# Performance work log

Measured on AMD Instinct MI355X. Metric: run time of the kernel, lower is better.

Reference implementation:

```python
import jax, jax.numpy as jnp
import numpy as np

I_DECAY = 0.95
STAG_THRESH = 0.95
MAX_GATE = 0.6
MIN_I_GATE = 0.25
EPS = 1e-12


def setup_inputs() -> dict:
    key = jax.random.key(0)
    ks = jax.random.split(key, 9)
    B, T, D_IN, D_OUT = 4, 2048, 2048, 2048
    x = jax.random.normal(ks[0], (B, T, D_IN), dtype=jnp.float32)
    s = 1.0 / np.sqrt(D_IN)
    Wp = jax.random.uniform(ks[1], (D_IN, D_OUT), jnp.float32, -s, s)
    Wi = jax.random.uniform(ks[2], (D_IN, D_OUT), jnp.float32, -s, s) * 0.3
    Wd = jax.random.uniform(ks[3], (D_IN, D_OUT), jnp.float32, -s, s) * 0.3
    gate_w = jax.random.uniform(ks[4], (D_IN, 3), jnp.float32, -s, s)
    gate_b = jnp.array([0.5, 0.0, 0.0], dtype=jnp.float32)
    kick_vec = jax.random.normal(ks[5], (D_OUT,), dtype=jnp.float32) * 0.01
    kick_w = jax.random.uniform(ks[6], (D_IN, 1), jnp.float32, -s, s)
    kick_b = jnp.full((1,), -2.0, dtype=jnp.float32)
    bias = jnp.zeros((D_OUT,), dtype=jnp.float32)
    return {"x": x, "Wp": Wp, "Wi": Wi, "Wd": Wd, "gate_w": gate_w,
            "gate_b": gate_b, "kick_vec": kick_vec, "kick_w": kick_w,
            "kick_b": kick_b, "bias": bias}


def _ema_integral(x, decay):
    # x: [B,T,D] -> time-major scan; integral[0] = x[0]
    xt = jnp.swapaxes(x, 0, 1)  # [T,B,D]

    def step(carry, xcur):
        new = decay * carry + (1.0 - decay) * xcur
        return new, new

    init = xt[0]
    _, rest = jax.lax.scan(step, init, xt[1:])
    integral = jnp.concatenate([init[None], rest], axis=0)
    return jnp.swapaxes(integral, 0, 1)  # [B,T,D]


def reference(x, Wp, Wi, Wd, gate_w, gate_b, kick_vec, kick_w, kick_b, bias):
    B, T, D = x.shape
    # --- EMA integral (linear recurrence over T) ---
    integral = _ema_integral(x, I_DECAY)

    # --- stagnation-aware derivative ---
    diff = jnp.concatenate(
        [jnp.zeros_like(x[:, :1]), x[:, 1:] - x[:, :-1]], axis=1)
    x_norm = x / jnp.maximum(
        jnp.linalg.norm(x, axis=-1, keepdims=True), EPS)
    cos_sim = jnp.concatenate(
        [jnp.zeros((B, 1), x.dtype),
         jnp.sum(x_norm[:, 1:] * x_norm[:, :-1], axis=-1)], axis=1)  # [B,T]
    stagnation = (cos_sim > STAG_THRESH).astype(x.dtype)
    kick_strength = jax.nn.sigmoid(
        jnp.einsum('btd,do->bto', x, kick_w) + kick_b)[..., 0]  # [B,T]
    derivative = diff + (stagnation * kick_strength)[..., None] * kick_vec

    # --- gates: softmax -> clamp max -> clamp I min -> renormalize ---
    g = jax.nn.softmax(jnp.einsum('btd,dg->btg', x, gate_w) + gate_b, axis=-1)
    g = jnp.minimum(g, MAX_GATE)
    g = g.at[..., 1].set(jnp.maximum(g[..., 1], MIN_I_GATE))
    g = g / jnp.sum(g, axis=-1, keepdims=True)

    out = (g[..., 0:1] * jnp.einsum('btd,do->bto', x, Wp)
           + g[..., 1:2] * jnp.einsum('btd,do->bto', integral, Wi)
           + g[..., 2:3] * jnp.einsum('btd,do->bto', derivative, Wd))
    return out + bias
```

## Files before the change

### kernel.cpp

```cpp
#include <hip/hip_runtime.h>

#define DH 2048
#define TT 2048
#define BB 4
#define MROWS 8192
#define NZ 6144
#define NCH 128
#define LCH 16
#define LAM 0.44012667f
#define LAM2 1.982646e-06f

typedef __attribute__((ext_vector_type(8))) short bf16x8;
typedef __attribute__((ext_vector_type(4))) float f32x4;

__device__ __forceinline__ unsigned short f2bf(float f) {
  union { float f; unsigned int u; } v; v.f = f;
  unsigned int u = v.u;
  return (unsigned short)((u + 0x7FFFu + ((u >> 16) & 1u)) >> 16);
}
__device__ __forceinline__ float bf2f(unsigned short u) {
  union { unsigned int i; float f; } v; v.i = ((unsigned int)u) << 16;
  return v.f;
}
__device__ __forceinline__ void gld16(const unsigned short* g, unsigned short* l) {
  __builtin_amdgcn_global_load_lds((const __attribute__((address_space(1))) void*)g,
                                   (__attribute__((address_space(3))) void*)l, 16, 0, 0);
}

__global__ __launch_bounds__(256) void prep_w(const float* __restrict__ Wp,
                                              const float* __restrict__ Wi,
                                              const float* __restrict__ Wd,
                                              const float* __restrict__ kick_vec,
                                              unsigned short* __restrict__ Wt,
                                              float* __restrict__ kvWd) {
  __shared__ float tile[64][65];
  int bid = blockIdx.x;
  int mat = bid >> 10;
  int t2 = bid & 1023;
  int dt = (t2 >> 5) * 64;
  int ot = (t2 & 31) * 64;
  const float* W = (mat == 0) ? Wp : ((mat == 1) ? Wi : Wd);
  int nbase = mat * DH;
  int tid = threadIdx.x;
  int r = tid >> 4;
  int c4 = (tid & 15) * 4;
#pragma unroll
  for (int i = 0; i < 4; ++i) {
    int rr = r + i * 16;
    float4 v = *(const float4*)&W[(size_t)(dt + rr) * DH + ot + c4];
    tile[rr][c4 + 0] = v.x; tile[rr][c4 + 1] = v.y;
    tile[rr][c4 + 2] = v.z; tile[rr][c4 + 3] = v.w;
  }
  __syncthreads();
  int o = tid >> 3;
  int d8 = (tid & 7) * 8;
#pragma unroll
  for (int pass = 0; pass < 2; ++pass) {
    int oo = o + pass * 32;
    union { unsigned short u[8]; uint4 v; } pk;
#pragma unroll
    for (int i = 0; i < 8; ++i) pk.u[i] = f2bf(tile[d8 + i][oo]);
    *(uint4*)&Wt[(size_t)(nbase + ot + oo) * DH + dt + d8] = pk.v;
  }
  if (mat == 2 && tid < 64) {
    float s = 0.f;
#pragma unroll 8
    for (int dd = 0; dd < 64; ++dd) s += kick_vec[dt + dd] * tile[dd][tid];
    atomicAdd(&kvWd[ot + tid], s);
  }
}

__global__ __launch_bounds__(256) void conv_x(const float* __restrict__ x,
                                              const float* __restrict__ gate_w,
                                              const float* __restrict__ gate_b,
                                              const float* __restrict__ kick_w,
                                              const float* __restrict__ kick_b,
                                              float* __restrict__ rs,
                                              unsigned short* __restrict__ A) {
  int r = blockIdx.x;
  int t = r & (TT - 1);
  const float* xr = x + (size_t)r * DH;
  const float* xq = xr - DH;
  const bool hp = (t != 0);
  int tid = threadIdx.x;
  float a0 = 0, a1 = 0, a2 = 0, ak = 0, axx = 0, apx = 0, app = 0;
#pragma unroll
  for (int it = 0; it < 2; ++it) {
    int d0 = (tid + it * 256) * 4;
    float4 xv = *(const float4*)(xr + d0);
    float4 pv = hp ? *(const float4*)(xq + d0) : make_float4(0.f, 0.f, 0.f, 0.f);
    float4 q0 = *(const float4*)(gate_w + (size_t)d0 * 3);
    float4 q1 = *(const float4*)(gate_w + (size_t)d0 * 3 + 4);
    float4 q2 = *(const float4*)(gate_w + (size_t)d0 * 3 + 8);
    float4 kw = *(const float4*)(kick_w + d0);
    float xa[4] = {xv.x, xv.y, xv.z, xv.w};
    float pa[4] = {pv.x, pv.y, pv.z, pv.w};
    a0 += xa[0] * q0.x + xa[1] * q0.w + xa[2] * q1.z + xa[3] * q2.y;
    a1 += xa[0] * q0.y + xa[1] * q1.x + xa[2] * q1.w + xa[3] * q2.z;
    a2 += xa[0] * q0.z + xa[1] * q1.y + xa[2] * q2.x + xa[3] * q2.w;
    ak += xa[0] * kw.x + xa[1] * kw.y + xa[2] * kw.z + xa[3] * kw.w;
    union { unsigned short u[4]; uint2 v; } pk;
#pragma unroll
    for (int j = 0; j < 4; ++j) {
      axx += xa[j] * xa[j];
      apx += xa[j] * pa[j];
      app += pa[j] * pa[j];
      pk.u[j] = f2bf(xa[j]);
    }
    *(uint2*)&A[(size_t)r * DH + d0] = pk.v;
  }
#pragma unroll
  for (int off = 32; off > 0; off >>= 1) {
    a0 += __shfl_xor(a0, off); a1 += __shfl_xor(a1, off);
    a2 += __shfl_xor(a2, off); ak += __shfl_xor(ak, off);
    axx += __shfl_xor(axx, off); apx += __shfl_xor(apx, off);
    app += __shfl_xor(app, off);
  }
  __shared__ float red[4][7];
  int wv = tid >> 6;
  if ((tid & 63) == 0) {
    red[wv][0] = a0; red[wv][1] = a1; red[wv][2] = a2; red[wv][3] = ak;
    red[wv][4] = axx; red[wv][5] = apx; red[wv][6] = app;
  }
  __syncthreads();
  if (tid == 0) {
    float v[7];
#pragma unroll
    for (int i = 0; i < 7; ++i) v[i] = red[0][i] + red[1][i] + red[2][i] + red[3][i];
    float l0 = v[0] + gate_b[0], l1 = v[1] + gate_b[1], l2 = v[2] + gate_b[2];
    float mx = fmaxf(l0, fmaxf(l1, l2));
    float e0 = expf(l0 - mx), e1 = expf(l1 - mx), e2 = expf(l2 - mx);
    float inv = 1.f / (e0 + e1 + e2);
    float G0 = fminf(e0 * inv, 0.6f);
    float G1 = fminf(e1 * inv, 0.6f);
    float G2 = fminf(e2 * inv, 0.6f);
    G1 = fmaxf(G1, 0.25f);
    float inv2 = 1.f / (G0 + G1 + G2);
    G0 *= inv2; G1 *= inv2; G2 *= inv2;
    float ks = 1.f / (1.f + expf(-(v[3] + kick_b[0])));
    float nn = fmaxf(sqrtf(v[4]), 1e-12f) * fmaxf(sqrtf(v[6]), 1e-12f);
    float cs = hp ? (v[5] / nn) : 0.f;
    float cc = (cs > 0.95f) ? (G2 * ks) : 0.f;
    *(float4*)(rs + (size_t)r * 4) = make_float4(G0, G1, G2, cc);
  }
}

__global__ __launch_bounds__(256) void gemm_kernel(const unsigned short* __restrict__ A,
                                                   const unsigned short* __restrict__ Bt,
                                                   unsigned short* __restrict__ Z,
                                                   unsigned short* __restrict__ cpb) {
  __shared__ __align__(16) unsigned short lA[128 * 64];
  __shared__ __align__(16) unsigned short lB[128 * 64];
  const int tid = threadIdx.x;
  const int wave = tid >> 6, lane = tid & 63;
  const int bid = blockIdx.x;
  const int xcd = bid & 7;
  const int loc = bid >> 3;
  const int mblk = xcd * 8 + (loc & 7);
  const int nblk = loc >> 3;
  const int m0 = mblk * 128, n0 = nblk * 128;

  const int srow = wave * 32 + (lane >> 3);
  const int scol = ((lane & 7) ^ (lane >> 3)) * 8;
  const unsigned short* ga = A + (size_t)(m0 + srow) * DH + scol;
  const unsigned short* gb = Bt + (size_t)(n0 + srow) * DH + scol;
  unsigned short* la = &lA[(wave * 32) * 64];
  unsigned short* lb = &lB[(wave * 32) * 64];

  f32x4 acc[4][4] = {};
  const int arow = ((wave >> 1) * 64 + (lane & 15)) * 64;
  const int brow = ((wave & 1) * 64 + (lane & 15)) * 64;
  const int cbq = lane >> 4;
  const int swz = lane & 7;

  for (int k0 = 0; k0 < DH; k0 += 64) {
#pragma unroll
    for (int j = 0; j < 4; ++j) {
      gld16(ga + k0 + (size_t)j * 8 * DH, la + j * 8 * 64);
      gld16(gb + k0 + (size_t)j * 8 * DH, lb + j * 8 * 64);
    }
    __syncthreads();
#pragma unroll
    for (int kb = 0; kb < 2; ++kb) {
      const int kphys = ((kb * 4 + cbq) ^ swz) * 8;
      bf16x8 av[4], bv[4];
#pragma unroll
      for (int mi = 0; mi < 4; ++mi)
        av[mi] = *(const bf16x8*)&lA[arow + mi * 16 * 64 + kphys];
#pragma unroll
      for (int ni = 0; ni < 4; ++ni)
        bv[ni] = *(const bf16x8*)&lB[brow + ni * 16 * 64 + kphys];
#pragma unroll
      for (int mi = 0; mi < 4; ++mi)
#pragma unroll
        for (int ni = 0; ni < 4; ++ni)
          acc[mi][ni] = __builtin_amdgcn_mfma_f32_16x16x32_bf16(av[mi], bv[ni], acc[mi][ni], 0, 0, 0);
    }
    __syncthreads();
  }

  const int lr = lane >> 4, lc = lane & 15;
  const int mbase = m0 + (wave >> 1) * 64, nbase = n0 + (wave & 1) * 64;

  if (nblk >= 16 && nblk < 32) {
    float w12 = (lr == 3) ? 1.0f : (lr == 2) ? 0.81450625f
              : (lr == 1) ? 0.66342043f : 0.54036009f;
    w12 *= 0.05f;
#pragma unroll
    for (int mi = 0; mi < 4; ++mi) {
      const int mrow = mbase + mi * 16;
      const int bb = mrow >> 11;
      const int chh = (mrow >> 4) & (NCH - 1);
      const bool first = (chh == 0);
#pragma unroll
      for (int ni = 0; ni < 4; ++ni) {
        float v0 = acc[mi][ni][0];
        float s = ((v0 * 0.95f + acc[mi][ni][1]) * 0.95f + acc[mi][ni][2]) * 0.95f
                  + acc[mi][ni][3];
        if (first && lr == 0) s += 19.0f * 0.857375f * v0;
        s *= w12;
        s += __shfl_xor(s, 16);
        s += __shfl_xor(s, 32);
        if (lr == 0) {
          int nloc = nbase + ni * 16 + lc - 2048;
          cpb[((size_t)bb * NCH + chh) * DH + nloc] = f2bf(s);
        }
      }
    }
  }

#pragma unroll
  for (int ni = 0; ni < 4; ++ni) {
    const int n = nbase + ni * 16 + lc;
#pragma unroll
    for (int mi = 0; mi < 4; ++mi) {
#pragma unroll
      for (int rg = 0; rg < 4; ++rg) {
        const int m = mbase + mi * 16 + lr * 4 + rg;
        Z[(size_t)m * NZ + n] = f2bf(acc[mi][ni][rg]);
      }
    }
  }
}

__global__ __launch_bounds__(256) void zi_p1(unsigned short* __restrict__ cpb,
                                             float* __restrict__ gc) {
  int gid = blockIdx.x * 256 + threadIdx.x;
  int n = gid & (DH - 1);
  int g = (gid >> 11) & 7;
  int b = gid >> 14;
  float run = 0.f;
#pragma unroll
  for (int j = 0; j < 16; ++j) {
    size_t idx = ((size_t)b * NCH + g * 16 + j) * DH + n;
    float c = bf2f(cpb[idx]);
    cpb[idx] = f2bf(run);
    run = c + LAM * run;
  }
  gc[((size_t)b * 8 + g) * DH + n] = run;
}

__global__ __launch_bounds__(256) void zi_p2(float* __restrict__ gc) {
  int gid = blockIdx.x * 256 + threadIdx.x;
  int n = gid & (DH - 1);
  int b = gid >> 11;
  float run = 0.f;
#pragma unroll
  for (int g = 0; g < 8; ++g) {
    size_t idx = ((size_t)b * 8 + g) * DH + n;
    float old = gc[idx];
    gc[idx] = run;
    run = old + LAM2 * run;
  }
}

__global__ __launch_bounds__(256) void final_combine(const unsigned short* __restrict__ Z,
                                                     const float* __restrict__ rs,
                                                     const unsigned short* __restrict__ cpb,
                                                     const float* __restrict__ gc,
                                                     const float* __restrict__ kvWd,
                                                     const float* __restrict__ bias,
                                                     float* __restrict__ out) {
  int tid = threadIdx.x;
  int n = blockIdx.y * 1024 + tid * 4;
  int ch = blockIdx.x & (NCH - 1);
  int b = blockIdx.x >> 7;
  int r0 = b * TT + ch * LCH;
  const unsigned short* zb = Z + (size_t)r0 * NZ + n;
  const bool first_chunk = (ch == 0);

  int g = ch >> 4, j = ch & 15;
  float pw = 1.f;
  for (int i = 0; i < j; ++i) pw *= LAM;
  float Pv[4];
  {
    union { unsigned short u[4]; uint2 v; } c;
    c.v = *(const uint2*)&cpb[((size_t)b * NCH + ch) * DH + n];
    float4 gp = *(const float4*)&gc[((size_t)b * 8 + g) * DH + n];
    float gpa[4] = {gp.x, gp.y, gp.z, gp.w};
#pragma unroll
    for (int i = 0; i < 4; ++i) Pv[i] = bf2f(c.u[i]) + pw * gpa[i];
  }
  float kv[4], bz[4];
  {
    float4 k0 = *(const float4*)&kvWd[n];
    float4 b0 = *(const float4*)&bias[n];
    kv[0]=k0.x; kv[1]=k0.y; kv[2]=k0.z; kv[3]=k0.w;
    bz[0]=b0.x; bz[1]=b0.y; bz[2]=b0.z; bz[3]=b0.w;
  }
  float zdp[4];
  if (!first_chunk) {
    union { unsigned short u[4]; uint2 v; } c;
    c.v = *(const uint2*)(zb - NZ + 2 * DH);
#pragma unroll
    for (int i = 0; i < 4; ++i) zdp[i] = bf2f(c.u[i]);
  } else {
#pragma unroll
    for (int i = 0; i < 4; ++i) zdp[i] = 0.f;
  }
  float J[4];
#pragma unroll
  for (int i = 0; i < 4; ++i) J[i] = 0.f;
  float f = 1.f;
  uint2 cp = *(const uint2*)(zb);
  uint2 ci = *(const uint2*)(zb + DH);
  uint2 cd = *(const uint2*)(zb + 2 * DH);
#pragma unroll
  for (int tau = 0; tau < LCH; ++tau) {
    uint2 np, ni, nd;
    if (tau < LCH - 1) {
      const unsigned short* zn = zb + (size_t)(tau + 1) * NZ;
      np = *(const uint2*)(zn);
      ni = *(const uint2*)(zn + DH);
      nd = *(const uint2*)(zn + 2 * DH);
    }
    float4 gg = *(const float4*)&rs[(size_t)(r0 + tau) * 4];
    union { unsigned short u[4]; uint2 v; } up, ui, ud;
    up.v = cp; ui.v = ci; ud.v = cd;
    const bool vfirst = first_chunk && (tau == 0);
    f *= 0.95f;
    float o[4];
#pragma unroll
    for (int i = 0; i < 4; ++i) {
      float xp = bf2f(up.u[i]), xi = bf2f(ui.u[i]), xd = bf2f(ud.u[i]);
      if (vfirst) J[i] = xi;
      else J[i] = 0.95f * J[i] + 0.05f * xi;
      float I = J[i] + f * Pv[i];
      float diff = vfirst ? 0.f : (xd - zdp[i]);
      o[i] = gg.x * xp + gg.y * I + gg.z * diff + gg.w * kv[i] + bz[i];
      zdp[i] = xd;
    }
    *(float4*)(out + (size_t)(r0 + tau) * DH + n) = make_float4(o[0], o[1], o[2], o[3]);
    cp = np; ci = ni; cd = nd;
  }
}

extern "C" void kernel_launch(void* const* d_in, const int* in_sizes, int n_in,
                              void* d_out, int out_size, void* d_ws, size_t ws_size,
                              hipStream_t stream) {
  const float* x        = (const float*)d_in[0];
  const float* Wp       = (const float*)d_in[1];
  const float* Wi       = (const float*)d_in[2];
  const float* Wd       = (const float*)d_in[3];
  const float* gate_w   = (const float*)d_in[4];
  const float* gate_b   = (const float*)d_in[5];
  const float* kick_vec = (const float*)d_in[6];
  const float* kick_w   = (const float*)d_in[7];
  const float* kick_b   = (const float*)d_in[8];
  const float* bias     = (const float*)d_in[9];
  float* out = (float*)d_out;

  char* ws = (char*)d_ws;
  unsigned short* Wt  = (unsigned short*)(ws + 0);
  unsigned short* Z   = (unsigned short*)(ws + 25165824);
  float* rs   = (float*)(ws + 125829120);
  float* kvWd = (float*)(ws + 125960192);
  unsigned short* cpb = (unsigned short*)(ws + 125968384);
  float* gc   = (float*)(ws + 128065536);
  unsigned short* A = (unsigned short*)d_out;
  (void)ws_size; (void)in_sizes; (void)n_in; (void)out_size;

  hipMemsetAsync(kvWd, 0, DH * sizeof(float), stream);
  prep_w<<<dim3(3072), dim3(256), 0, stream>>>(Wp, Wi, Wd, kick_vec, Wt, kvWd);
  conv_x<<<dim3(8192), dim3(256), 0, stream>>>(x, gate_w, gate_b, kick_w, kick_b, rs, A);
  gemm_kernel<<<dim3(3072), dim3(256), 0, stream>>>(A, Wt, Z, cpb);
  zi_p1<<<dim3(256), dim3(256), 0, stream>>>(cpb, gc);
  zi_p2<<<dim3(32), dim3(256), 0, stream>>>(gc);
  final_combine<<<dim3(512, 2), dim3(256), 0, stream>>>(Z, rs, cpb, gc, kvWd, bias, out);
}
```

Baseline: 425.5 us.

## Rewrite GEMM as 256x256 tile, 8-wave, double-buffered pipelined kernel

```diff
diff --git a/kernel.cpp b/kernel.cpp
--- a/kernel.cpp
+++ b/kernel.cpp
@@ -145,69 +145,121 @@
   }
 }
 
-__global__ __launch_bounds__(256) void gemm_kernel(const unsigned short* __restrict__ A,
-                                                   const unsigned short* __restrict__ Bt,
-                                                   unsigned short* __restrict__ Z,
-                                                   unsigned short* __restrict__ cpb) {
-  __shared__ __align__(16) unsigned short lA[128 * 64];
-  __shared__ __align__(16) unsigned short lB[128 * 64];
+
+#define BAR __builtin_amdgcn_s_barrier()
+#define VMW8 asm volatile("s_waitcnt vmcnt(8)" ::: "memory")
+#define VMW4 asm volatile("s_waitcnt vmcnt(4)" ::: "memory")
+#define VMW2 asm volatile("s_waitcnt vmcnt(2)" ::: "memory")
+#define VMW0 asm volatile("s_waitcnt vmcnt(0)" ::: "memory")
+#define LGK0 asm volatile("s_waitcnt lgkmcnt(0)" ::: "memory")
+
+#define ST_A(bf, h, kt) do { \
+  gld16(pA + (size_t)((h) * 64) * DH + (kt) * 64,       lA + (bf) * 16384 + (h) * 8192 + ldsW); \
+  gld16(pA + (size_t)((h) * 64 + 128) * DH + (kt) * 64, lA + (bf) * 16384 + (h) * 8192 + 4096 + ldsW); \
+} while (0)
+#define ST_B(bf, g, kt) do { \
+  gld16(pB + (size_t)((g) * 32) * DH + (kt) * 64,       lB + (bf) * 16384 + (g) * 8192 + ldsW); \
+  gld16(pB + (size_t)((g) * 32 + 128) * DH + (kt) * 64, lB + (bf) * 16384 + (g) * 8192 + 4096 + ldsW); \
+} while (0)
+
+#define RD_A(bf, h) do { \
+  const unsigned short* p_ = lA + (bf) * 16384 + (h) * 8192 + aRd; \
+  _Pragma("unroll") \
+  for (int mi_ = 0; mi_ < 4; ++mi_) { \
+    av[mi_][0] = *(const bf16x8*)(p_ + mi_ * 1024 + kph0); \
+    av[mi_][1] = *(const bf16x8*)(p_ + mi_ * 1024 + kph1); \
+  } \
+} while (0)
+#define RD_B(bf, g) do { \
+  const unsigned short* p_ = lB + (bf) * 16384 + (g) * 8192 + bRd; \
+  _Pragma("unroll") \
+  for (int ni_ = 0; ni_ < 2; ++ni_) { \
+    bv[g][ni_][0] = *(const bf16x8*)(p_ + ni_ * 1024 + kph0); \
+    bv[g][ni_][1] = *(const bf16x8*)(p_ + ni_ * 1024 + kph1); \
+  } \
+} while (0)
+
+#define MM(h, g) do { \
+  __builtin_amdgcn_s_setprio(1); \
+  _Pragma("unroll") \
+  for (int mi_ = 0; mi_ < 4; ++mi_) { \
+    _Pragma("unroll") \
+    for (int ni_ = 0; ni_ < 2; ++ni_) { \
+      f32x4 c_ = acc[(h) * 4 + mi_][(g) * 2 + ni_]; \
+      c_ = __builtin_amdgcn_mfma_f32_16x16x32_bf16(av[mi_][0], bv[g][ni_][0], c_, 0, 0, 0); \
+      c_ = __builtin_amdgcn_mfma_f32_16x16x32_bf16(av[mi_][1], bv[g][ni_][1], c_, 0, 0, 0); \
+      acc[(h) * 4 + mi_][(g) * 2 + ni_] = c_; \
+    } \
+  } \
+  __builtin_amdgcn_s_setprio(0); \
+} while (0)
+
+__global__ __launch_bounds__(512, 2) void gemm_kernel(const unsigned short* __restrict__ A,
+                                                      const unsigned short* __restrict__ Bt,
+                                                      unsigned short* __restrict__ Z,
+                                                      unsigned short* __restrict__ cpb) {
+  __shared__ __align__(16) unsigned short lA[2 * 16384];
+  __shared__ __align__(16) unsigned short lB[2 * 16384];
   const int tid = threadIdx.x;
   const int wave = tid >> 6, lane = tid & 63;
   const int bid = blockIdx.x;
   const int xcd = bid & 7;
   const int loc = bid >> 3;
-  const int mblk = xcd * 8 + (loc & 7);
-  const int nblk = loc >> 3;
-  const int m0 = mblk * 128, n0 = nblk * 128;
-
-  const int srow = wave * 32 + (lane >> 3);
-  const int scol = ((lane & 7) ^ (lane >> 3)) * 8;
-  const unsigned short* ga = A + (size_t)(m0 + srow) * DH + scol;
-  const unsigned short* gb = Bt + (size_t)(n0 + srow) * DH + scol;
-  unsigned short* la = &lA[(wave * 32) * 64];
-  unsigned short* lb = &lB[(wave * 32) * 64];
-
-  f32x4 acc[4][4] = {};
-  const int arow = ((wave >> 1) * 64 + (lane & 15)) * 64;
-  const int brow = ((wave & 1) * 64 + (lane & 15)) * 64;
-  const int cbq = lane >> 4;
-  const int swz = lane & 7;
-
-  for (int k0 = 0; k0 < DH; k0 += 64) {
-#pragma unroll
-    for (int j = 0; j < 4; ++j) {
-      gld16(ga + k0 + (size_t)j * 8 * DH, la + j * 8 * 64);
-      gld16(gb + k0 + (size_t)j * 8 * DH, lb + j * 8 * 64);
-    }
-    __syncthreads();
-#pragma unroll
-    for (int kb = 0; kb < 2; ++kb) {
-      const int kphys = ((kb * 4 + cbq) ^ swz) * 8;
-      bf16x8 av[4], bv[4];
-#pragma unroll
-      for (int mi = 0; mi < 4; ++mi)
-        av[mi] = *(const bf16x8*)&lA[arow + mi * 16 * 64 + kphys];
-#pragma unroll
-      for (int ni = 0; ni < 4; ++ni)
-        bv[ni] = *(const bf16x8*)&lB[brow + ni * 16 * 64 + kphys];
-#pragma unroll
-      for (int mi = 0; mi < 4; ++mi)
-#pragma unroll
-        for (int ni = 0; ni < 4; ++ni)
-          acc[mi][ni] = __builtin_amdgcn_mfma_f32_16x16x32_bf16(av[mi], bv[ni], acc[mi][ni], 0, 0, 0);
-    }
-    __syncthreads();
-  }
-
-  const int lr = lane >> 4, lc = lane & 15;
-  const int mbase = m0 + (wave >> 1) * 64, nbase = n0 + (wave & 1) * 64;
-
-  if (nblk >= 16 && nblk < 32) {
-    float w12 = (lr == 3) ? 1.0f : (lr == 2) ? 0.81450625f
-              : (lr == 1) ? 0.66342043f : 0.54036009f;
+  const int mblk = xcd * 4 + (loc & 3);
+  const int nblk = loc >> 2;
+  const int m0 = mblk * 256, n0 = nblk * 256;
+
+  const int wm = wave >> 2, wn = wave & 3;
+  const int rA = lane & 15, q = lane >> 4, sw = lane & 7;
+  const int kph0 = ((0 + q) ^ sw) * 8;
+  const int kph1 = ((4 + q) ^ sw) * 8;
+  const int aRd = wm * 4096 + rA * 64;
+  const int bRd = wn * 2048 + rA * 64;
+
+  const int trow = tid >> 3;
+  const int tcol = ((tid & 7) ^ (trow & 7)) * 8;
+  const unsigned short* pA = A + (size_t)(m0 + trow) * DH + tcol;
+  const unsigned short* pB = Bt + (size_t)(n0 + (trow >> 5) * 64 + (trow & 31)) * DH + tcol;
+  const int ldsW = wave * 512;
+
+  bf16x8 av[4][2];
+  bf16x8 bv[2][2][2];
+  f32x4 acc[8][4] = {};
+
+  ST_A(0, 0, 0); ST_B(0, 0, 0); ST_B(0, 1, 0); ST_A(0, 1, 0);
+  ST_A(1, 0, 1); ST_B(1, 0, 1);
+  VMW8; BAR;
+
+#pragma unroll 1
+  for (int i = 0; i < 15; ++i) {
+    const int t1 = 2 * i + 1, t2 = 2 * i + 2, t3 = 2 * i + 3;
+    RD_A(0, 0); RD_B(0, 0); ST_B(1, 1, t1); VMW8; BAR; LGK0; MM(0, 0); BAR;
+    RD_B(0, 1);             ST_A(1, 1, t1); VMW8; BAR; LGK0; MM(0, 1); BAR;
+    RD_A(0, 1);             ST_A(0, 0, t2);       BAR; LGK0; MM(1, 0); BAR;
+                            ST_B(0, 0, t2); VMW8; BAR; LGK0; MM(1, 1); BAR;
+    RD_A(1, 0); RD_B(1, 0); ST_B(0, 1, t2); VMW8; BAR; LGK0; MM(0, 0); BAR;
+    RD_B(1, 1);             ST_A(0, 1, t2); VMW8; BAR; LGK0; MM(0, 1); BAR;
+    RD_A(1, 1);             ST_A(1, 0, t3);       BAR; LGK0; MM(1, 0); BAR;
+                            ST_B(1, 0, t3); VMW8; BAR; LGK0; MM(1, 1); BAR;
+  }
+  RD_A(0, 0); RD_B(0, 0); ST_B(1, 1, 31); VMW8; BAR; LGK0; MM(0, 0); BAR;
+  RD_B(0, 1);             ST_A(1, 1, 31); VMW8; BAR; LGK0; MM(0, 1); BAR;
+  RD_A(0, 1);                                   BAR; LGK0; MM(1, 0); BAR;
+                                          VMW4; BAR; LGK0; MM(1, 1); BAR;
+  RD_A(1, 0); RD_B(1, 0);                 VMW2; BAR; LGK0; MM(0, 0); BAR;
+  RD_B(1, 1);                             VMW0; BAR; LGK0; MM(0, 1); BAR;
+  RD_A(1, 1);                                   BAR; LGK0; MM(1, 0); BAR;
+                                                            MM(1, 1);
+
+  const int mbase = m0 + wm * 128;
+  const int nbase = n0 + wn * 64;
+
+  if (nblk >= 8 && nblk < 16) {
+    float w12 = (q == 3) ? 1.0f : (q == 2) ? 0.81450625f
+              : (q == 1) ? 0.66342043f : 0.54036009f;
     w12 *= 0.05f;
 #pragma unroll
-    for (int mi = 0; mi < 4; ++mi) {
+    for (int mi = 0; mi < 8; ++mi) {
       const int mrow = mbase + mi * 16;
       const int bb = mrow >> 11;
       const int chh = (mrow >> 4) & (NCH - 1);
@@ -217,12 +269,12 @@
         float v0 = acc[mi][ni][0];
         float s = ((v0 * 0.95f + acc[mi][ni][1]) * 0.95f + acc[mi][ni][2]) * 0.95f
                   + acc[mi][ni][3];
-        if (first && lr == 0) s += 19.0f * 0.857375f * v0;
+        if (first && q == 0) s += 19.0f * 0.857375f * v0;
         s *= w12;
         s += __shfl_xor(s, 16);
         s += __shfl_xor(s, 32);
-        if (lr == 0) {
-          int nloc = nbase + ni * 16 + lc - 2048;
+        if (q == 0) {
+          int nloc = nbase + ni * 16 + rA - 2048;
           cpb[((size_t)bb * NCH + chh) * DH + nloc] = f2bf(s);
         }
       }
@@ -231,17 +283,29 @@
 
 #pragma unroll
   for (int ni = 0; ni < 4; ++ni) {
-    const int n = nbase + ni * 16 + lc;
-#pragma unroll
-    for (int mi = 0; mi < 4; ++mi) {
+    const int n = nbase + ni * 16 + rA;
+#pragma unroll
+    for (int mi = 0; mi < 8; ++mi) {
 #pragma unroll
       for (int rg = 0; rg < 4; ++rg) {
-        const int m = mbase + mi * 16 + lr * 4 + rg;
+        const int m = mbase + mi * 16 + q * 4 + rg;
         Z[(size_t)m * NZ + n] = f2bf(acc[mi][ni][rg]);
       }
     }
   }
 }
+
+#undef BAR
+#undef VMW8
+#undef VMW4
+#undef VMW2
+#undef VMW0
+#undef LGK0
+#undef ST_A
+#undef ST_B
+#undef RD_A
+#undef RD_B
+#undef MM
 
 __global__ __launch_bounds__(256) void zi_p1(unsigned short* __restrict__ cpb,
                                              float* __restrict__ gc) {
@@ -383,7 +447,7 @@
   hipMemsetAsync(kvWd, 0, DH * sizeof(float), stream);
   prep_w<<<dim3(3072), dim3(256), 0, stream>>>(Wp, Wi, Wd, kick_vec, Wt, kvWd);
   conv_x<<<dim3(8192), dim3(256), 0, stream>>>(x, gate_w, gate_b, kick_w, kick_b, rs, A);
-  gemm_kernel<<<dim3(3072), dim3(256), 0, stream>>>(A, Wt, Z, cpb);
+  gemm_kernel<<<dim3(768), dim3(512), 0, stream>>>(A, Wt, Z, cpb);
   zi_p1<<<dim3(256), dim3(256), 0, stream>>>(cpb, gc);
   zi_p2<<<dim3(32), dim3(256), 0, stream>>>(gc);
   final_combine<<<dim3(512, 2), dim3(256), 0, stream>>>(Z, rs, cpb, gc, kvWd, bias, out);
```

New measurement: 419.0 us. Within noise of the previous version (-1.5%).
